# Optimization experiments

Measured on AMD Instinct MI355X. Metric: run time of the kernel, lower is better.

Reference implementation:

```python
import jax, jax.numpy as jnp
import numpy as np

N_VARS = 50000   # number of variables (graph nodes)
N_TX = 200000    # number of transforms in the bucket (edges)
D = 32           # per-variable slice size (layout.sizes[v])


def setup_inputs() -> dict:
    key = jax.random.key(0)
    k1, k2, k3, k4, k5 = jax.random.split(key, 5)
    theta = jax.random.normal(k1, (N_VARS * D,), dtype=jnp.float32)  # flat variable buffer
    # stacked_params of one TransformBucket: per-transform Linear(D, D)
    W = jax.random.normal(k2, (N_TX, D, D), dtype=jnp.float32) / np.sqrt(D)
    b = jax.random.normal(k3, (N_TX, D), dtype=jnp.float32)
    src_ids = jax.random.randint(k4, (N_TX,), 0, N_VARS)  # gather_indices rows (var id -> slice)
    tgt_ids = jax.random.randint(k5, (N_TX,), 0, N_VARS)  # scatter_indices rows
    return {"theta": theta, "W": W, "b": b, "src_ids": src_ids, "tgt_ids": tgt_ids}


def reference(theta, W, b, src_ids, tgt_ids):
    # Flat buffer viewed as [n_vars, D]; each variable slice is contiguous per Layout.
    tv = theta.reshape(N_VARS, D)
    # Bucketized gather: pull src slices for every transform in the bucket. [E, D]
    x = tv[src_ids]
    # vmapped transform application (stacked Linear params). [E, D]
    preds_e = jnp.einsum("eij,ej->ei", W, x) + b
    # Scatter-reduce predictions back into shared flat layout. [n_vars, D]
    preds = jnp.zeros_like(tv).at[tgt_ids].add(preds_e)
    # Energy residual per variable slice (gaussian energy: 0.5*||theta - pred||^2).
    resid = tv - preds
    return resid.reshape(-1)
```

## Files before the change

### kernel.cpp

```cpp
#include <hip/hip_runtime.h>

#define N_VARS 50000
#define N_TX   200000
#define DSZ    32

__global__ void copy_theta_kernel(const float4* __restrict__ theta,
                                  float4* __restrict__ out, int n4) {
    int i = blockIdx.x * blockDim.x + threadIdx.x;
    int stride = gridDim.x * blockDim.x;
    for (; i < n4; i += stride) out[i] = theta[i];
}

__global__ void transform_scatter_kernel(const float* __restrict__ theta,
                                         const float* __restrict__ W,
                                         const float* __restrict__ b,
                                         const int* __restrict__ src,
                                         const int* __restrict__ tgt,
                                         float* __restrict__ out) {
    const int lane   = threadIdx.x & 63;
    const int waveId = (blockIdx.x * blockDim.x + threadIdx.x) >> 6;
    const int nWaves = (gridDim.x * blockDim.x) >> 6;
    const int j0     = (lane & 7) << 2;
    const int rsub   = lane >> 3;

    for (int e = waveId; e < N_TX; e += nWaves) {
        const int s = src[e];
        const int t = tgt[e];

        const float4 xv = *reinterpret_cast<const float4*>(theta + (size_t)s * DSZ + j0);

        const float* We = W + (size_t)e * (DSZ * DSZ);
        const float* be = b + (size_t)e * DSZ;
        float* oute = out + (size_t)t * DSZ;

        #pragma unroll
        for (int it = 0; it < 4; ++it) {
            const float4 wv =
                *reinterpret_cast<const float4*>(We + it * 256 + lane * 4);
            float p = wv.x * xv.x + wv.y * xv.y + wv.z * xv.z + wv.w * xv.w;
            p += __shfl_xor(p, 1);
            p += __shfl_xor(p, 2);
            p += __shfl_xor(p, 4);
            if ((lane & 7) == 0) {
                const int i = it * 8 + rsub;
                const float y = p + be[i];
                atomicAdd(&oute[i], -y);
            }
        }
    }
}

extern "C" void kernel_launch(void* const* d_in, const int* in_sizes, int n_in,
                              void* d_out, int out_size, void* d_ws, size_t ws_size,
                              hipStream_t stream) {
    const float* theta = (const float*)d_in[0];
    const float* W     = (const float*)d_in[1];
    const float* b     = (const float*)d_in[2];
    const int*   src   = (const int*)d_in[3];
    const int*   tgt   = (const int*)d_in[4];
    float* out = (float*)d_out;

    const int n4 = (N_VARS * DSZ) / 4;
    const int cpBlocks = 1024;
    copy_theta_kernel<<<cpBlocks, 256, 0, stream>>>(
        (const float4*)theta, (float4*)out, n4);

    const int txBlocks = 2048;
    transform_scatter_kernel<<<txBlocks, 256, 0, stream>>>(
        theta, W, b, src, tgt, out);
}
```

Before: 192.2 us.

## Process two transforms per wave with contiguous chunks and nontemporal W loads

Gives each wave a contiguous chunk of 26 transforms instead of a grid-stride loop, and unrolls two transforms per iteration. All four W rows are issued up front as nontemporal loads so more bytes are in flight, and bias loads are hoisted ahead of the reductions. The atomic writes are spread across lanes so 32 lanes each add one row, rather than 8 lanes doing four serialized rounds. The kernel is bound by streaming W, so the aim is more memory-level parallelism, at the cost of more registers and a grid sized from the chunk length.

```diff
diff --git a/kernel.cpp b/kernel.cpp
--- a/kernel.cpp
+++ b/kernel.cpp
@@ -3,6 +3,8 @@
 #define N_VARS 50000
 #define N_TX   200000
 #define DSZ    32
+
+typedef float f32x4 __attribute__((ext_vector_type(4)));
 
 __global__ void copy_theta_kernel(const float4* __restrict__ theta,
                                   float4* __restrict__ out, int n4) {
@@ -11,41 +13,99 @@
     for (; i < n4; i += stride) out[i] = theta[i];
 }
 
-__global__ void transform_scatter_kernel(const float* __restrict__ theta,
-                                         const float* __restrict__ W,
-                                         const float* __restrict__ b,
-                                         const int* __restrict__ src,
-                                         const int* __restrict__ tgt,
-                                         float* __restrict__ out) {
-    const int lane   = threadIdx.x & 63;
-    const int waveId = (blockIdx.x * blockDim.x + threadIdx.x) >> 6;
-    const int nWaves = (gridDim.x * blockDim.x) >> 6;
-    const int j0     = (lane & 7) << 2;
-    const int rsub   = lane >> 3;
+__global__ __launch_bounds__(256)
+void transform_scatter_kernel(const float* __restrict__ theta,
+                              const float* __restrict__ W,
+                              const float* __restrict__ bia,
+                              const int* __restrict__ src,
+                              const int* __restrict__ tgt,
+                              float* __restrict__ out) {
+    const int CHUNK = 26;
+    const int lane = threadIdx.x & 63;
+    const int wave = (blockIdx.x * blockDim.x + threadIdx.x) >> 6;
 
-    for (int e = waveId; e < N_TX; e += nWaves) {
-        const int s = src[e];
-        const int t = tgt[e];
+    int e0 = wave * CHUNK;
+    if (e0 >= N_TX) return;
+    const int e1 = (e0 + CHUNK < N_TX) ? e0 + CHUNK : N_TX;
 
-        const float4 xv = *reinterpret_cast<const float4*>(theta + (size_t)s * DSZ + j0);
+    const int j0    = (lane & 7) << 2;
+    const int g     = lane >> 3;
+    const bool wr   = (lane & 7) < 4;
+    const int myIt  = lane & 3;
+    const int myRow = myIt * 8 + g;
 
-        const float* We = W + (size_t)e * (DSZ * DSZ);
-        const float* be = b + (size_t)e * DSZ;
-        float* oute = out + (size_t)t * DSZ;
+    int e = e0;
+    for (; e + 1 < e1; e += 2) {
+        const int sA = src[e],     tA = tgt[e];
+        const int sB = src[e + 1], tB = tgt[e + 1];
+
+        const f32x4 xA = *reinterpret_cast<const f32x4*>(theta + (size_t)sA * DSZ + j0);
+        const f32x4 xB = *reinterpret_cast<const f32x4*>(theta + (size_t)sB * DSZ + j0);
+
+        const f32x4* WA = reinterpret_cast<const f32x4*>(W + (size_t)e * (DSZ * DSZ));
+        const f32x4* WB = WA + 256;
+
+        const f32x4 a0 = __builtin_nontemporal_load(WA +   0 + lane);
+        const f32x4 a1 = __builtin_nontemporal_load(WA +  64 + lane);
+        const f32x4 a2 = __builtin_nontemporal_load(WA + 128 + lane);
+        const f32x4 a3 = __builtin_nontemporal_load(WA + 192 + lane);
+        const f32x4 c0 = __builtin_nontemporal_load(WB +   0 + lane);
+        const f32x4 c1 = __builtin_nontemporal_load(WB +  64 + lane);
+        const f32x4 c2 = __builtin_nontemporal_load(WB + 128 + lane);
+        const f32x4 c3 = __builtin_nontemporal_load(WB + 192 + lane);
+
+        const float biasA = bia[(size_t)e * DSZ + myRow];
+        const float biasB = bia[(size_t)(e + 1) * DSZ + myRow];
+
+        float pA0 = a0.x * xA.x + a0.y * xA.y + a0.z * xA.z + a0.w * xA.w;
+        float pA1 = a1.x * xA.x + a1.y * xA.y + a1.z * xA.z + a1.w * xA.w;
+        float pA2 = a2.x * xA.x + a2.y * xA.y + a2.z * xA.z + a2.w * xA.w;
+        float pA3 = a3.x * xA.x + a3.y * xA.y + a3.z * xA.z + a3.w * xA.w;
+        float pB0 = c0.x * xB.x + c0.y * xB.y + c0.z * xB.z + c0.w * xB.w;
+        float pB1 = c1.x * xB.x + c1.y * xB.y + c1.z * xB.z + c1.w * xB.w;
+        float pB2 = c2.x * xB.x + c2.y * xB.y + c2.z * xB.z + c2.w * xB.w;
+        float pB3 = c3.x * xB.x + c3.y * xB.y + c3.z * xB.z + c3.w * xB.w;
 
         #pragma unroll
-        for (int it = 0; it < 4; ++it) {
-            const float4 wv =
-                *reinterpret_cast<const float4*>(We + it * 256 + lane * 4);
-            float p = wv.x * xv.x + wv.y * xv.y + wv.z * xv.z + wv.w * xv.w;
-            p += __shfl_xor(p, 1);
-            p += __shfl_xor(p, 2);
-            p += __shfl_xor(p, 4);
-            if ((lane & 7) == 0) {
-                const int i = it * 8 + rsub;
-                const float y = p + be[i];
-                atomicAdd(&oute[i], -y);
-            }
+        for (int m = 1; m <= 4; m <<= 1) {
+            pA0 += __shfl_xor(pA0, m); pA1 += __shfl_xor(pA1, m);
+            pA2 += __shfl_xor(pA2, m); pA3 += __shfl_xor(pA3, m);
+            pB0 += __shfl_xor(pB0, m); pB1 += __shfl_xor(pB1, m);
+            pB2 += __shfl_xor(pB2, m); pB3 += __shfl_xor(pB3, m);
+        }
+
+        if (wr) {
+            const float vA = (myIt == 0) ? pA0 : (myIt == 1) ? pA1 : (myIt == 2) ? pA2 : pA3;
+            const float vB = (myIt == 0) ? pB0 : (myIt == 1) ? pB1 : (myIt == 2) ? pB2 : pB3;
+            atomicAdd(out + (size_t)tA * DSZ + myRow, -(vA + biasA));
+            atomicAdd(out + (size_t)tB * DSZ + myRow, -(vB + biasB));
+        }
+    }
+
+    for (; e < e1; ++e) {
+        const int s = src[e], t = tgt[e];
+        const f32x4 xv = *reinterpret_cast<const f32x4*>(theta + (size_t)s * DSZ + j0);
+        const f32x4* We = reinterpret_cast<const f32x4*>(W + (size_t)e * (DSZ * DSZ));
+        const float biasv = bia[(size_t)e * DSZ + myRow];
+        float p0, p1, p2, p3;
+        {
+            const f32x4 a0 = __builtin_nontemporal_load(We +   0 + lane);
+            const f32x4 a1 = __builtin_nontemporal_load(We +  64 + lane);
+            const f32x4 a2 = __builtin_nontemporal_load(We + 128 + lane);
+            const f32x4 a3 = __builtin_nontemporal_load(We + 192 + lane);
+            p0 = a0.x * xv.x + a0.y * xv.y + a0.z * xv.z + a0.w * xv.w;
+            p1 = a1.x * xv.x + a1.y * xv.y + a1.z * xv.z + a1.w * xv.w;
+            p2 = a2.x * xv.x + a2.y * xv.y + a2.z * xv.z + a2.w * xv.w;
+            p3 = a3.x * xv.x + a3.y * xv.y + a3.z * xv.z + a3.w * xv.w;
+        }
+        #pragma unroll
+        for (int m = 1; m <= 4; m <<= 1) {
+            p0 += __shfl_xor(p0, m); p1 += __shfl_xor(p1, m);
+            p2 += __shfl_xor(p2, m); p3 += __shfl_xor(p3, m);
+        }
+        if (wr) {
+            const float v = (myIt == 0) ? p0 : (myIt == 1) ? p1 : (myIt == 2) ? p2 : p3;
+            atomicAdd(out + (size_t)t * DSZ + myRow, -(v + biasv));
         }
     }
 }
@@ -61,11 +121,10 @@
     float* out = (float*)d_out;
 
     const int n4 = (N_VARS * DSZ) / 4;
-    const int cpBlocks = 1024;
-    copy_theta_kernel<<<cpBlocks, 256, 0, stream>>>(
-        (const float4*)theta, (float4*)out, n4);
+    copy_theta_kernel<<<1024, 256, 0, stream>>>((const float4*)theta, (float4*)out, n4);
 
-    const int txBlocks = 2048;
-    transform_scatter_kernel<<<txBlocks, 256, 0, stream>>>(
-        theta, W, b, src, tgt, out);
+    const int CHUNK = 26;
+    const int nWaves = (N_TX + CHUNK - 1) / CHUNK;
+    const int blocks = (nWaves + 3) / 4;
+    transform_scatter_kernel<<<blocks, 256, 0, stream>>>(theta, W, b, src, tgt, out);
 }
```

Result: faster. 164.9 us (-14.2%).
